# Kernel optimization log

Measured on AMD Instinct MI355X. Metric: run time of the kernel, lower is better.

## Reference

```python
import jax, jax.numpy as jnp
import numpy as np

# Fixed (non-trainable) 3x3 line-feature kernels, ordered j=0..3 as in the torch module
_KERNELS = np.array([
    [[0.0, 0.0, 0.0], [-0.5, 1.0, -0.5], [0.0, 0.0, 0.0]],   # kernel0 (horizontal)
    [[0.0, 0.0, -0.5], [0.0, 1.0, 0.0], [-0.5, 0.0, 0.0]],   # kernel1 (anti-diagonal)
    [[0.0, -0.5, 0.0], [0.0, 1.0, 0.0], [0.0, -0.5, 0.0]],   # kernel2 (vertical)
    [[-0.5, 0.0, 0.0], [0.0, 1.0, 0.0], [0.0, 0.0, -0.5]],   # kernel3 (diagonal)
], dtype=np.float32)

_EPS = 1e-5  # torch InstanceNorm2d default eps


def setup_inputs() -> dict:
    key = jax.random.key(0)
    x = jax.random.normal(key, (32, 4, 512, 512), dtype=jnp.float32)
    return {"x": x}


def reference(x):
    B, C, H, W = x.shape
    kernels = jnp.asarray(_KERNELS)  # [4, 3, 3]
    out = jnp.zeros_like(x)
    for j in range(4):  # fixed small structural loop over 4 distinct kernels
        w = jnp.broadcast_to(kernels[j][None, None], (C, 1, 3, 3))  # depthwise: groups=C
        y = jax.lax.conv_general_dilated(
            x, w,
            window_strides=(1, 1),
            padding=[(1, 1), (1, 1)],
            dimension_numbers=("NCHW", "OIHW", "NCHW"),
            feature_group_count=C,
        )
        out = out + ((y + 1.0) * 0.5) * (float(2 ** j) / 15.0)
    # InstanceNorm2d (no affine): normalize per (b, c) over spatial dims, biased variance
    mean = jnp.mean(out, axis=(2, 3), keepdims=True)
    var = jnp.var(out, axis=(2, 3), keepdims=True)
    return (out - mean) * jax.lax.rsqrt(var + _EPS)
```

## Files before the change

### kernel.cpp

```cpp
#include <hip/hip_runtime.h>


#define H 512
#define W 512
#define PLANES 128
#define NBLOCKS (PLANES * 8)
#define MAGIC 0x5EED5EEDu

typedef float vfloat4 __attribute__((ext_vector_type(4)));

#define WT0 (-8.0f/30.0f)
#define WT1 (-4.0f/30.0f)
#define WT2 (-2.0f/30.0f)
#define WM  (-1.0f/30.0f)

__device__ __forceinline__ void wload2(const float* __restrict__ rowp, int lane, bool valid,
                                       float& lA, float4& mA, float& rA,
                                       float& lB, float4& mB, float& rB) {
    if (valid) {
        mA = *reinterpret_cast<const float4*>(rowp + lane * 4);
        mB = *reinterpret_cast<const float4*>(rowp + 256 + lane * 4);
    } else {
        mA = make_float4(0.0f, 0.0f, 0.0f, 0.0f);
        mB = make_float4(0.0f, 0.0f, 0.0f, 0.0f);
    }
    float upA = __shfl_up(mA.w, 1);
    float dnA = __shfl_down(mA.x, 1);
    float upB = __shfl_up(mB.w, 1);
    float dnB = __shfl_down(mB.x, 1);
    float c255 = __shfl(mA.w, 63);
    float c256 = __shfl(mB.x, 0);
    lA = (lane == 0)  ? 0.0f : upA;
    rA = (lane == 63) ? c256 : dnA;
    lB = (lane == 0)  ? c255 : upB;
    rB = (lane == 63) ? 0.0f : dnB;
}

__device__ __forceinline__ float4 conv_row(float al, float4 a, float ar,
                                           float bl, float4 b, float br,
                                           float dl, float4 d, float dr) {
    float4 o;
    o.x = b.x + WT0*(al  + d.y) + WT1*(a.x + d.x) + WT2*(a.y + dl ) + WM*(bl  + b.y);
    o.y = b.y + WT0*(a.x + d.z) + WT1*(a.y + d.y) + WT2*(a.z + d.x) + WM*(b.x + b.z);
    o.z = b.z + WT0*(a.y + d.w) + WT1*(a.z + d.z) + WT2*(a.w + d.y) + WM*(b.y + b.w);
    o.w = b.w + WT0*(a.z + dr ) + WT1*(a.w + d.w) + WT2*(ar  + d.z) + WM*(b.z + br );
    return o;
}

__global__ __launch_bounds__(256, 4) void fused_kernel(const float* __restrict__ x,
                                                       float* __restrict__ ws,
                                                       float* __restrict__ out) {
    const int tid   = threadIdx.x;
    const int wid   = tid >> 6;
    const int lane  = tid & 63;
    const int plane = blockIdx.x >> 3;
    const int slab  = blockIdx.x & 7;
    const int r0    = slab * 64 + wid * 16;
    const int c0A   = lane * 4;
    const int c0B   = 256 + lane * 4;

    const float* __restrict__ p = x + (size_t)plane * H * W;

    float alA, arA, blA, brA, dlA, drA;
    float alB, arB, blB, brB, dlB, drB;
    float4 aA, bA, dA, aB, bB, dB;

    wload2(p + (size_t)(r0 - 1) * W, lane, r0 > 0, alA, aA, arA, alB, aB, arB);
    wload2(p + (size_t)r0 * W,       lane, true,   blA, bA, brA, blB, bB, brB);

    float s = 0.0f, ss = 0.0f;
    for (int r = r0; r < r0 + 16; ++r) {
        wload2(p + (size_t)(r + 1) * W, lane, (r + 1) < H, dlA, dA, drA, dlB, dB, drB);
        float4 oA = conv_row(alA, aA, arA, blA, bA, brA, dlA, dA, drA);
        float4 oB = conv_row(alB, aB, arB, blB, bB, brB, dlB, dB, drB);
        s  += ((oA.x + oA.y) + (oA.z + oA.w)) + ((oB.x + oB.y) + (oB.z + oB.w));
        ss += ((oA.x*oA.x + oA.y*oA.y) + (oA.z*oA.z + oA.w*oA.w))
            + ((oB.x*oB.x + oB.y*oB.y) + (oB.z*oB.z + oB.w*oB.w));
        alA = blA; aA = bA; arA = brA;  alB = blB; aB = bB; arB = brB;
        blA = dlA; bA = dA; brA = drA;  blB = dlB; bB = dB; brB = drB;
    }

    for (int off = 32; off > 0; off >>= 1) {
        s  += __shfl_down(s,  off);
        ss += __shfl_down(ss, off);
    }
    __shared__ float sh[8];
    if (lane == 0) { sh[wid * 2] = s; sh[wid * 2 + 1] = ss; }
    __syncthreads();

    unsigned int* flags = reinterpret_cast<unsigned int*>(ws + 2 * NBLOCKS);
    if (tid == 0) {
        ws[blockIdx.x * 2 + 0] = (sh[0] + sh[2]) + (sh[4] + sh[6]);
        ws[blockIdx.x * 2 + 1] = (sh[1] + sh[3]) + (sh[5] + sh[7]);
        __hip_atomic_store(&flags[blockIdx.x], MAGIC,
                           __ATOMIC_RELEASE, __HIP_MEMORY_SCOPE_AGENT);
    }

    wload2(p + (size_t)(r0 - 1) * W, lane, r0 > 0, alA, aA, arA, alB, aB, arB);
    wload2(p + (size_t)r0 * W,       lane, true,   blA, bA, brA, blB, bB, brB);

    __shared__ float sb[2];
    if (tid < 64) {
        float s2 = 0.0f, ss2 = 0.0f;
        if (lane < 8) {
            const int idx = plane * 8 + lane;
            while (__hip_atomic_load(&flags[idx], __ATOMIC_ACQUIRE,
                                     __HIP_MEMORY_SCOPE_AGENT) != MAGIC) {
                __builtin_amdgcn_s_sleep(2);
            }
            s2  = ws[idx * 2 + 0];
            ss2 = ws[idx * 2 + 1];
        }
        for (int off = 4; off > 0; off >>= 1) {
            s2  += __shfl_down(s2,  off);
            ss2 += __shfl_down(ss2, off);
        }
        if (lane == 0) { sb[0] = s2; sb[1] = ss2; }
    }
    __syncthreads();

    const float invN = 1.0f / (float)(H * W);
    const float mean = sb[0] * invN;
    const float var  = sb[1] * invN - mean * mean;
    const float rstd = rsqrtf(var + 4e-5f);

    float* __restrict__ q = out + (size_t)plane * H * W;

    for (int r = r0; r < r0 + 16; ++r) {
        wload2(p + (size_t)(r + 1) * W, lane, (r + 1) < H, dlA, dA, drA, dlB, dB, drB);
        float4 oA = conv_row(alA, aA, arA, blA, bA, brA, dlA, dA, drA);
        float4 oB = conv_row(alB, aB, arB, blB, bB, brB, dlB, dB, drB);
        vfloat4 yA, yB;
        yA.x = (oA.x - mean) * rstd;
        yA.y = (oA.y - mean) * rstd;
        yA.z = (oA.z - mean) * rstd;
        yA.w = (oA.w - mean) * rstd;
        yB.x = (oB.x - mean) * rstd;
        yB.y = (oB.y - mean) * rstd;
        yB.z = (oB.z - mean) * rstd;
        yB.w = (oB.w - mean) * rstd;
        __builtin_nontemporal_store(yA, reinterpret_cast<vfloat4*>(q + (size_t)r * W + c0A));
        __builtin_nontemporal_store(yB, reinterpret_cast<vfloat4*>(q + (size_t)r * W + c0B));
        alA = blA; aA = bA; arA = brA;  alB = blB; aB = bB; arB = brB;
        blA = dlA; bA = dA; brA = drA;  blB = dlB; bB = dB; brB = drB;
    }
}

extern "C" void kernel_launch(void* const* d_in, const int* in_sizes, int n_in,
                              void* d_out, int out_size, void* d_ws, size_t ws_size,
                              hipStream_t stream) {
    const float* x = (const float*)d_in[0];
    float* out = (float*)d_out;
    float* ws  = (float*)d_ws;

    fused_kernel<<<dim3(NBLOCKS), dim3(256), 0, stream>>>(x, ws, out);
}
```

Before: 282.4 us.

## Split fused spin-wait kernel into separate stats and normalize kernels

Replaces the single persistent-style kernel, which used global flag spin-waits between blocks of a plane, with two launches: one computes per-slab sums and sums of squares, the other reduces them and writes the normalized output. It also doubles the block count, with each warp covering 8 rows, fully unrolls the row loops and raises the occupancy hint. This removes the inter-block spin synchronization and its reliance on co-residency. The cost is an extra kernel launch and a second pass over the input, which may no longer be in cache when the second kernel reads it.

```diff
diff --git a/kernel.cpp b/kernel.cpp
--- a/kernel.cpp
+++ b/kernel.cpp
@@ -4,8 +4,7 @@
 #define H 512
 #define W 512
 #define PLANES 128
-#define NBLOCKS (PLANES * 8)
-#define MAGIC 0x5EED5EEDu
+#define NBLOCKS (PLANES * 16)
 
 typedef float vfloat4 __attribute__((ext_vector_type(4)));
 
@@ -47,17 +46,14 @@
     return o;
 }
 
-__global__ __launch_bounds__(256, 4) void fused_kernel(const float* __restrict__ x,
-                                                       float* __restrict__ ws,
-                                                       float* __restrict__ out) {
+__global__ __launch_bounds__(256, 8) void stats_kernel(const float* __restrict__ x,
+                                                       float* __restrict__ ws) {
     const int tid   = threadIdx.x;
     const int wid   = tid >> 6;
     const int lane  = tid & 63;
-    const int plane = blockIdx.x >> 3;
-    const int slab  = blockIdx.x & 7;
-    const int r0    = slab * 64 + wid * 16;
-    const int c0A   = lane * 4;
-    const int c0B   = 256 + lane * 4;
+    const int plane = blockIdx.x >> 4;
+    const int slab  = blockIdx.x & 15;
+    const int r0    = slab * 32 + wid * 8;
 
     const float* __restrict__ p = x + (size_t)plane * H * W;
 
@@ -69,7 +65,8 @@
     wload2(p + (size_t)r0 * W,       lane, true,   blA, bA, brA, blB, bB, brB);
 
     float s = 0.0f, ss = 0.0f;
-    for (int r = r0; r < r0 + 16; ++r) {
+    #pragma unroll
+    for (int r = r0; r < r0 + 8; ++r) {
         wload2(p + (size_t)(r + 1) * W, lane, (r + 1) < H, dlA, dA, drA, dlB, dB, drB);
         float4 oA = conv_row(alA, aA, arA, blA, bA, brA, dlA, dA, drA);
         float4 oB = conv_row(alB, aB, arB, blB, bB, brB, dlB, dB, drB);
@@ -87,38 +84,46 @@
     __shared__ float sh[8];
     if (lane == 0) { sh[wid * 2] = s; sh[wid * 2 + 1] = ss; }
     __syncthreads();
-
-    unsigned int* flags = reinterpret_cast<unsigned int*>(ws + 2 * NBLOCKS);
     if (tid == 0) {
         ws[blockIdx.x * 2 + 0] = (sh[0] + sh[2]) + (sh[4] + sh[6]);
         ws[blockIdx.x * 2 + 1] = (sh[1] + sh[3]) + (sh[5] + sh[7]);
-        __hip_atomic_store(&flags[blockIdx.x], MAGIC,
-                           __ATOMIC_RELEASE, __HIP_MEMORY_SCOPE_AGENT);
     }
+}
 
+__global__ __launch_bounds__(256, 8) void norm_kernel(const float* __restrict__ x,
+                                                      const float* __restrict__ ws,
+                                                      float* __restrict__ out) {
+    const int tid   = threadIdx.x;
+    const int wid   = tid >> 6;
+    const int lane  = tid & 63;
+    const int plane = blockIdx.x >> 4;
+    const int slab  = blockIdx.x & 15;
+    const int r0    = slab * 32 + wid * 8;
+    const int c0A   = lane * 4;
+    const int c0B   = 256 + lane * 4;
+
+    const float* __restrict__ p = x + (size_t)plane * H * W;
+
+    float alA, arA, blA, brA, dlA, drA;
+    float alB, arB, blB, brB, dlB, drB;
+    float4 aA, bA, dA, aB, bB, dB;
     wload2(p + (size_t)(r0 - 1) * W, lane, r0 > 0, alA, aA, arA, alB, aB, arB);
     wload2(p + (size_t)r0 * W,       lane, true,   blA, bA, brA, blB, bB, brB);
 
     __shared__ float sb[2];
     if (tid < 64) {
-        float s2 = 0.0f, ss2 = 0.0f;
-        if (lane < 8) {
-            const int idx = plane * 8 + lane;
-            while (__hip_atomic_load(&flags[idx], __ATOMIC_ACQUIRE,
-                                     __HIP_MEMORY_SCOPE_AGENT) != MAGIC) {
-                __builtin_amdgcn_s_sleep(2);
-            }
-            s2  = ws[idx * 2 + 0];
-            ss2 = ws[idx * 2 + 1];
+        float s = 0.0f, ss = 0.0f;
+        if (lane < 16) {
+            s  = ws[(plane * 16 + lane) * 2 + 0];
+            ss = ws[(plane * 16 + lane) * 2 + 1];
         }
-        for (int off = 4; off > 0; off >>= 1) {
-            s2  += __shfl_down(s2,  off);
-            ss2 += __shfl_down(ss2, off);
+        for (int off = 8; off > 0; off >>= 1) {
+            s  += __shfl_down(s,  off);
+            ss += __shfl_down(ss, off);
         }
-        if (lane == 0) { sb[0] = s2; sb[1] = ss2; }
+        if (lane == 0) { sb[0] = s; sb[1] = ss; }
     }
     __syncthreads();
-
     const float invN = 1.0f / (float)(H * W);
     const float mean = sb[0] * invN;
     const float var  = sb[1] * invN - mean * mean;
@@ -126,7 +131,8 @@
 
     float* __restrict__ q = out + (size_t)plane * H * W;
 
-    for (int r = r0; r < r0 + 16; ++r) {
+    #pragma unroll
+    for (int r = r0; r < r0 + 8; ++r) {
         wload2(p + (size_t)(r + 1) * W, lane, (r + 1) < H, dlA, dA, drA, dlB, dB, drB);
         float4 oA = conv_row(alA, aA, arA, blA, bA, brA, dlA, dA, drA);
         float4 oB = conv_row(alB, aB, arB, blB, bB, brB, dlB, dB, drB);
@@ -153,5 +159,6 @@
     float* out = (float*)d_out;
     float* ws  = (float*)d_ws;
 
-    fused_kernel<<<dim3(NBLOCKS), dim3(256), 0, stream>>>(x, ws, out);
+    stats_kernel<<<dim3(NBLOCKS), dim3(256), 0, stream>>>(x, ws);
+    norm_kernel <<<dim3(NBLOCKS), dim3(256), 0, stream>>>(x, ws, out);
 }
```

New measurement: 460.9 us. 63.2% more time.
